# Kernel optimization log

Hardware: AMD Instinct MI355X
Metric: run time of the kernel (lower is better)

Reference implementation:

```python
import jax, jax.numpy as jnp
import numpy as np

N_HEAD, D_MODEL, D_HEAD = 16, 1024, 64
BSZ, SEQ = 4, 2048
SCALE = 1.0 / D_HEAD ** 0.5
LN_EPS = 1e-5
NEG = -1e10


def layer_norm(x, gamma, beta):
    mu = jnp.mean(x, axis=-1, keepdims=True)
    var = jnp.var(x, axis=-1, keepdims=True)
    return (x - mu) * jax.lax.rsqrt(var + LN_EPS) * gamma + beta


def setup_inputs() -> dict:
    key = jax.random.key(0)
    ks = jax.random.split(key, 8)
    q = jax.random.normal(ks[0], (BSZ, SEQ, D_MODEL), dtype=jnp.float32)
    attn_mask = jax.random.randint(ks[1], (SEQ, SEQ), 0, 2).astype(bool)
    s = 1.0 / np.sqrt(D_MODEL)
    Wq = jax.random.normal(ks[2], (D_MODEL, N_HEAD * D_HEAD), dtype=jnp.float32) * s
    Wk = jax.random.normal(ks[3], (D_MODEL, N_HEAD * D_HEAD), dtype=jnp.float32) * s
    Wv = jax.random.normal(ks[4], (D_MODEL, N_HEAD * D_HEAD), dtype=jnp.float32) * s
    Wo = jax.random.normal(ks[5], (N_HEAD * D_HEAD, D_MODEL), dtype=jnp.float32) * s
    gamma = jnp.ones((D_MODEL,), dtype=jnp.float32)
    beta = jnp.zeros((D_MODEL,), dtype=jnp.float32)
    return {"q": q, "attn_mask": attn_mask, "Wq": Wq, "Wk": Wk, "Wv": Wv,
            "Wo": Wo, "gamma": gamma, "beta": beta}


def reference(q, attn_mask, Wq, Wk, Wv, Wo, gamma, beta):
    # pre_lnorm: residual uses the normalized q (as in the torch code, q is reassigned)
    qn = layer_norm(q, gamma, beta)                      # (b, n1, d_model)
    hq = (qn @ Wq).reshape(BSZ, SEQ, N_HEAD, D_HEAD)     # self-attn: k = v = q
    hk = (qn @ Wk).reshape(BSZ, SEQ, N_HEAD, D_HEAD)
    hv = (qn @ Wv).reshape(BSZ, SEQ, N_HEAD, D_HEAD)
    score = jnp.einsum('bind,bjnd->ijbn', hq, hk) * SCALE  # (n1, n2, b, h)
    score = jnp.where(attn_mask[:, :, None, None], NEG, score)
    prob = jax.nn.softmax(score, axis=1)
    vec = jnp.einsum('ijbn,bjnd->bind', prob, hv).reshape(BSZ, SEQ, N_HEAD * D_HEAD)
    attn_out = vec @ Wo
    return qn + attn_out
```

## Files before the change

kernel.cpp:

```cpp
#include <hip/hip_runtime.h>

typedef __bf16 bf16;
typedef __bf16 bf16x8 __attribute__((ext_vector_type(8)));
typedef __bf16 bf16x4 __attribute__((ext_vector_type(4)));
typedef float  f32x4  __attribute__((ext_vector_type(4)));

#define MFMA16 __builtin_amdgcn_mfma_f32_16x16x32_bf16

static constexpr int   BSZ   = 4;
static constexpr int   SEQL  = 2048;
static constexpr int   DM    = 1024;
static constexpr int   NHEAD = 16;
static constexpr int   DHEAD = 64;
static constexpr float NEGB  = -16384.0f;
static constexpr float SCL2  = 0.125f * 1.44269504f;

__device__ __forceinline__ void glds16(bf16* lds, const bf16* g) {
    __builtin_amdgcn_global_load_lds(
        (const __attribute__((address_space(1))) unsigned int*)g,
        (__attribute__((address_space(3))) unsigned int*)lds, 16, 0, 0);
}

__global__ void detect_mask(const unsigned int* __restrict__ m, int* __restrict__ flag) {
    __shared__ int ok[4];
    if (threadIdx.x < 4) ok[threadIdx.x] = 1;
    __syncthreads();
    for (int i = 0; i < 16; ++i) {
        unsigned int w = m[threadIdx.x * 16 + i];
        if (!(w == 0u || w == 1u)) ok[0] = 0;
        if (w & 0xFEFEFEFEu) ok[1] = 0;
        if (!(w == 0u || w == 0x3F800000u)) ok[2] = 0;
        unsigned lo = w & 0xFFFFu, hi = w >> 16;
        if (!((lo == 0u || lo == 0x3F80u) && (hi == 0u || hi == 0x3F80u))) ok[3] = 0;
    }
    __syncthreads();
    if (threadIdx.x == 0)
        *flag = ok[0] ? 0 : (ok[1] ? 1 : (ok[2] ? 2 : 3));
}

__device__ __forceinline__ bool mask_at(const void* m, int fl, long idx) {
    if (fl == 0) return ((const int*)m)[idx] != 0;
    if (fl == 1) return ((const unsigned char*)m)[idx] != 0;
    if (fl == 2) return ((const float*)m)[idx] != 0.0f;
    return ((const unsigned short*)m)[idx] != 0;
}

__global__ __launch_bounds__(256) void prep_bits(const void* __restrict__ mask,
                                                 const int* __restrict__ flagp,
                                                 unsigned long long* __restrict__ mb) {
    const int fl = *flagp;
    const int word = blockIdx.x * 4 + (threadIdx.x >> 6);
    const long base = (long)word * 64 + (threadIdx.x & 63);
    unsigned long long b = __ballot(mask_at(mask, fl, base));
    if ((threadIdx.x & 63) == 0) mb[word] = b;
}

__global__ __launch_bounds__(256) void ln_kernel(
    const float* __restrict__ x, const float* __restrict__ g,
    const float* __restrict__ bta, bf16* __restrict__ y)
{
    const int row = blockIdx.x, t = threadIdx.x;
    const float4 v = ((const float4*)(x + (size_t)row * DM))[t];
    float s  = v.x + v.y + v.z + v.w;
    float ss = v.x * v.x + v.y * v.y + v.z * v.z + v.w * v.w;
    for (int m = 32; m >= 1; m >>= 1) { s += __shfl_xor(s, m); ss += __shfl_xor(ss, m); }
    __shared__ float red[8];
    const int w = t >> 6, L = t & 63;
    if (L == 0) { red[w] = s; red[4 + w] = ss; }
    __syncthreads();
    s  = red[0] + red[1] + red[2] + red[3];
    ss = red[4] + red[5] + red[6] + red[7];
    const float mu = s * (1.0f / DM);
    const float var = ss * (1.0f / DM) - mu * mu;
    const float r = rsqrtf(var + 1e-5f);
    const float4 gv = ((const float4*)g)[t];
    const float4 bv = ((const float4*)bta)[t];
    bf16x4 o;
    o[0] = (bf16)((v.x - mu) * r * gv.x + bv.x);
    o[1] = (bf16)((v.y - mu) * r * gv.y + bv.y);
    o[2] = (bf16)((v.z - mu) * r * gv.z + bv.z);
    o[3] = (bf16)((v.w - mu) * r * gv.w + bv.w);
    ((bf16x4*)(y + (size_t)row * DM))[t] = o;
}

__global__ void cvt_w(const float* __restrict__ Wq, const float* __restrict__ Wk,
                      const float* __restrict__ Wv, const float* __restrict__ Wo,
                      bf16* __restrict__ Wt)
{
    __shared__ float tile[32][33];
    const int z = blockIdx.z;
    const float* src = (z == 0) ? Wq : (z == 1) ? Wk : (z == 2) ? Wv : Wo;
    const float scl = (z == 1) ? SCL2 : 1.0f;
    bf16* dst = Wt + (size_t)z * DM * DM;
    const int tx = threadIdx.x, ty = threadIdx.y;
    const int nIn = blockIdx.x * 32 + tx;
    const int kIn = blockIdx.y * 32;
    for (int i = 0; i < 32; i += 8)
        tile[ty + i][tx] = src[(size_t)(kIn + ty + i) * DM + nIn];
    __syncthreads();
    const int nOut = blockIdx.x * 32;
    const int kOut = blockIdx.y * 32 + tx;
    for (int i = 0; i < 32; i += 8)
        dst[(size_t)(nOut + ty + i) * DM + kOut] = (bf16)(tile[tx][ty + i] * scl);
}

__device__ __forceinline__ void gemm128_core(
    const bf16* __restrict__ A, const bf16* __restrict__ Bt,
    int m0, int n0, bool swapped, f32x4 acc[4][4], bf16* Asm, bf16* Bsm)
{
    const int t = threadIdx.x, w = t >> 6, L = t & 63;
    const int lr = L & 15, lq = L >> 4;
    const int wm = w & 1, wn = w >> 1;
    const int srow = L >> 2, scol = (L & 3) * 8;
    const bf16* Ab = A  + (size_t)(m0 + w * 32 + srow) * DM + scol;
    const bf16* Bb = Bt + (size_t)(n0 + w * 32 + srow) * DM + scol;
    bf16* AsmW = Asm + (w * 32) * 32;
    bf16* BsmW = Bsm + (w * 32) * 32;
    for (int kk = 0; kk < DM; kk += 32) {
        __syncthreads();
        glds16(AsmW,           Ab + kk);
        glds16(AsmW + 16 * 32, Ab + (size_t)16 * DM + kk);
        glds16(BsmW,           Bb + kk);
        glds16(BsmW + 16 * 32, Bb + (size_t)16 * DM + kk);
        __syncthreads();
        bf16x8 af[4], bf_[4];
        #pragma unroll
        for (int i = 0; i < 4; ++i)
            af[i] = *(const bf16x8*)(Asm + (wm * 64 + i * 16 + lr) * 32 + lq * 8);
        #pragma unroll
        for (int j = 0; j < 4; ++j)
            bf_[j] = *(const bf16x8*)(Bsm + (wn * 64 + j * 16 + lr) * 32 + lq * 8);
        if (!swapped) {
            #pragma unroll
            for (int i = 0; i < 4; ++i)
                #pragma unroll
                for (int j = 0; j < 4; ++j)
                    acc[i][j] = MFMA16(af[i], bf_[j], acc[i][j], 0, 0, 0);
        } else {
            #pragma unroll
            for (int i = 0; i < 4; ++i)
                #pragma unroll
                for (int j = 0; j < 4; ++j)
                    acc[i][j] = MFMA16(bf_[j], af[i], acc[i][j], 0, 0, 0);
        }
    }
}

__global__ __launch_bounds__(256) void qkv128(
    const bf16* __restrict__ qn, const bf16* __restrict__ Wt,
    bf16* __restrict__ Qb, bf16* __restrict__ Kb, bf16* __restrict__ Vtb)
{
    __shared__ __align__(16) bf16 Asm[128 * 32];
    __shared__ __align__(16) bf16 Bsm[128 * 32];
    const int ny = blockIdx.y;
    const int z = ny >> 3;
    const int m0 = blockIdx.x * 128, n0 = (ny & 7) * 128;
    f32x4 acc[4][4] = {};
    gemm128_core(qn, Wt + (size_t)z * DM * DM, m0, n0, z == 2, acc, Asm, Bsm);
    const int t = threadIdx.x, L = t & 63, w = t >> 6;
    const int wm = w & 1, wn = w >> 1, lr = L & 15, lq = L >> 4;
    if (z < 2) {
        bf16* dst = z ? Kb : Qb;
        #pragma unroll
        for (int i = 0; i < 4; ++i)
            #pragma unroll
            for (int j = 0; j < 4; ++j)
                #pragma unroll
                for (int r = 0; r < 4; ++r) {
                    int m = m0 + wm * 64 + i * 16 + lq * 4 + r;
                    int n = n0 + wn * 64 + j * 16 + lr;
                    int b = m >> 11, s = m & 2047, h = n >> 6, d = n & 63;
                    dst[(((size_t)b * NHEAD + h) * SEQL + s) * DHEAD + d] = (bf16)acc[i][j][r];
                }
    } else {
        #pragma unroll
        for (int i = 0; i < 4; ++i)
            #pragma unroll
            for (int j = 0; j < 4; ++j)
                #pragma unroll
                for (int r = 0; r < 4; ++r) {
                    int dg = n0 + wn * 64 + j * 16 + lq * 4 + r;
                    int sg = m0 + wm * 64 + i * 16 + lr;
                    int h = dg >> 6, d = dg & 63, b = sg >> 11, s = sg & 2047;
                    Vtb[(((size_t)b * NHEAD + h) * DHEAD + d) * SEQL + s] = (bf16)acc[i][j][r];
                }
    }
}

__global__ __launch_bounds__(256) void out128(
    const bf16* __restrict__ vec, const bf16* __restrict__ Wot,
    const bf16* __restrict__ qnb, float* __restrict__ out)
{
    __shared__ __align__(16) bf16 Asm[128 * 32];
    __shared__ __align__(16) bf16 Bsm[128 * 32];
    const int m0 = blockIdx.x * 128, n0 = blockIdx.y * 128;
    f32x4 acc[4][4] = {};
    gemm128_core(vec, Wot, m0, n0, false, acc, Asm, Bsm);
    const int t = threadIdx.x, L = t & 63, w = t >> 6;
    const int wm = w & 1, wn = w >> 1, lr = L & 15, lq = L >> 4;
    #pragma unroll
    for (int i = 0; i < 4; ++i)
        #pragma unroll
        for (int j = 0; j < 4; ++j)
            #pragma unroll
            for (int r = 0; r < 4; ++r) {
                int m = m0 + wm * 64 + i * 16 + lq * 4 + r;
                int n = n0 + wn * 64 + j * 16 + lr;
                size_t idx = (size_t)m * DM + n;
                out[idx] = acc[i][j][r] + (float)qnb[idx];
            }
}

__global__ __launch_bounds__(256) void flash_attn(
    const bf16* __restrict__ Qb, const bf16* __restrict__ Kb,
    const bf16* __restrict__ Vtb, const unsigned long long* __restrict__ mb,
    bf16* __restrict__ vec)
{
    __shared__ __align__(16) bf16 Ksm [2][64 * 72];
    __shared__ __align__(16) bf16 Vtsm[2][64 * 72];

    const int t = threadIdx.x, w = t >> 6, L = t & 63;
    const int lr = L & 15, lq = L >> 4;
    const int bid = blockIdx.x;
    const int slot = bid & 7, rest = bid >> 3;
    const int qblk = rest & 15;
    const int bh = ((rest >> 4) << 3) + slot;
    const int b = bh >> 4, h = bh & 15;
    const int q0 = qblk * 128 + w * 32;

    const bf16* Qh  = Qb  + (size_t)bh * SEQL * DHEAD;
    const bf16* Kh  = Kb  + (size_t)bh * SEQL * DHEAD;
    const bf16* Vth = Vtb + (size_t)bh * DHEAD * SEQL;

    bf16x8 qf[2][2];
    #pragma unroll
    for (int qg = 0; qg < 2; ++qg)
        #pragma unroll
        for (int ks = 0; ks < 2; ++ks)
            qf[qg][ks] = *(const bf16x8*)(Qh + (size_t)(q0 + qg * 16 + lr) * DHEAD + ks * 32 + lq * 8);

    const unsigned long long* mrow0 = mb + (size_t)(q0 + lr) * (SEQL / 64);
    const unsigned long long* mrow1 = mb + (size_t)(q0 + 16 + lr) * (SEQL / 64);

    f32x4 o[4][2] = {};
    f32x4 lacc[2] = {};

    const bf16 one = (bf16)1.0f;
    const bf16x8 ones8 = {one, one, one, one, one, one, one, one};

    const int sr = t >> 2, sc = (t & 3) * 16;
    const int zrow = ((sr >> 2) & 1) * 32 + ((sr >> 5) & 1) * 16 + ((sr >> 3) & 3) * 4 + (sr & 3);
    constexpr int NT = SEQL / 64;
    bf16x8 kreg[2], vreg[2];

    kreg[0] = *(const bf16x8*)(Kh  + (size_t)sr * DHEAD + sc);
    kreg[1] = *(const bf16x8*)(Kh  + (size_t)sr * DHEAD + sc + 8);
    vreg[0] = *(const bf16x8*)(Vth + (size_t)sr * SEQL + sc);
    vreg[1] = *(const bf16x8*)(Vth + (size_t)sr * SEQL + sc + 8);
    *(bf16x8*)(Ksm[0]  + zrow * 72 + sc)     = kreg[0];
    *(bf16x8*)(Ksm[0]  + zrow * 72 + sc + 8) = kreg[1];
    *(bf16x8*)(Vtsm[0] + sr * 72 + sc)       = vreg[0];
    *(bf16x8*)(Vtsm[0] + sr * 72 + sc + 8)   = vreg[1];
    kreg[0] = *(const bf16x8*)(Kh  + (size_t)(64 + sr) * DHEAD + sc);
    kreg[1] = *(const bf16x8*)(Kh  + (size_t)(64 + sr) * DHEAD + sc + 8);
    vreg[0] = *(const bf16x8*)(Vth + (size_t)sr * SEQL + 64 + sc);
    vreg[1] = *(const bf16x8*)(Vth + (size_t)sr * SEQL + 64 + sc + 8);
    __syncthreads();

    for (int kt = 0; kt < NT; ++kt) {
        const int cur = kt & 1;
        const bf16* Kc = Ksm[cur];
        const bf16* Vc = Vtsm[cur];

        f32x4 s[4][2] = {};
        #pragma unroll
        for (int ks = 0; ks < 2; ++ks) {
            bf16x8 kf[4];
            #pragma unroll
            for (int jj = 0; jj < 4; ++jj)
                kf[jj] = *(const bf16x8*)(Kc + (jj * 16 + lr) * 72 + ks * 32 + lq * 8);
            #pragma unroll
            for (int jj = 0; jj < 4; ++jj)
                #pragma unroll
                for (int qg = 0; qg < 2; ++qg)
                    s[jj][qg] = MFMA16(kf[jj], qf[qg][ks], s[jj][qg], 0, 0, 0);
        }

        if (kt + 1 < NT) {
            bf16* Ka = Ksm[cur ^ 1];
            bf16* Va = Vtsm[cur ^ 1];
            *(bf16x8*)(Ka + zrow * 72 + sc)     = kreg[0];
            *(bf16x8*)(Ka + zrow * 72 + sc + 8) = kreg[1];
            *(bf16x8*)(Va + sr * 72 + sc)       = vreg[0];
            *(bf16x8*)(Va + sr * 72 + sc + 8)   = vreg[1];
            if (kt + 2 < NT) {
                const int kb2 = (kt + 2) * 64;
                kreg[0] = *(const bf16x8*)(Kh  + (size_t)(kb2 + sr) * DHEAD + sc);
                kreg[1] = *(const bf16x8*)(Kh  + (size_t)(kb2 + sr) * DHEAD + sc + 8);
                vreg[0] = *(const bf16x8*)(Vth + (size_t)sr * SEQL + kb2 + sc);
                vreg[1] = *(const bf16x8*)(Vth + (size_t)sr * SEQL + kb2 + sc + 8);
            }
        }

        bf16x8 pf[2][2];
        #pragma unroll
        for (int qg = 0; qg < 2; ++qg) {
            const unsigned long long wmk = (qg == 0 ? mrow0 : mrow1)[kt];
            const unsigned lo = (unsigned)(wmk >> (lq * 8));
            const unsigned hi = (unsigned)(wmk >> 32) >> (lq * 8);
            #pragma unroll
            for (int ks = 0; ks < 2; ++ks) {
                const unsigned na = (ks == 0 ? lo : hi) & 15u;
                const unsigned nb = ((ks == 0 ? lo : hi) >> 4) & 15u;
                bf16x8 pv;
                #pragma unroll
                for (int r = 0; r < 4; ++r) {
                    pv[r]     = (bf16)__builtin_amdgcn_exp2f(((na >> r) & 1u) ? NEGB : s[ks][qg][r]);
                    pv[4 + r] = (bf16)__builtin_amdgcn_exp2f(((nb >> r) & 1u) ? NEGB : s[2 + ks][qg][r]);
                }
                pf[qg][ks] = pv;
            }
        }

        #pragma unroll
        for (int ks = 0; ks < 2; ++ks) {
            #pragma unroll
            for (int qg = 0; qg < 2; ++qg)
                lacc[qg] = MFMA16(ones8, pf[qg][ks], lacc[qg], 0, 0, 0);
            #pragma unroll
            for (int dg = 0; dg < 4; ++dg) {
                bf16x8 vf = *(const bf16x8*)(Vc + (dg * 16 + lr) * 72 + ks * 32 + lq * 8);
                #pragma unroll
                for (int qg = 0; qg < 2; ++qg)
                    o[dg][qg] = MFMA16(vf, pf[qg][ks], o[dg][qg], 0, 0, 0);
            }
        }

        if (kt + 1 < NT) __syncthreads();
    }

    #pragma unroll
    for (int qg = 0; qg < 2; ++qg) {
        const float rl = 1.0f / lacc[qg][0];
        const size_t rowb = ((size_t)b * SEQL + q0 + qg * 16 + lr) * DM + h * DHEAD;
        #pragma unroll
        for (int dg = 0; dg < 4; ++dg) {
            bf16x4 ov;
            #pragma unroll
            for (int r = 0; r < 4; ++r) ov[r] = (bf16)(o[dg][qg][r] * rl);
            *(bf16x4*)(vec + rowb + dg * 16 + lq * 4) = ov;
        }
    }
}

extern "C" void kernel_launch(void* const* d_in, const int* in_sizes, int n_in,
                              void* d_out, int out_size, void* d_ws, size_t ws_size,
                              hipStream_t stream)
{
    const float* qin   = (const float*)d_in[0];
    const void*  mask  = d_in[1];
    const float* Wq    = (const float*)d_in[2];
    const float* Wk    = (const float*)d_in[3];
    const float* Wv    = (const float*)d_in[4];
    const float* Wo    = (const float*)d_in[5];
    const float* gamma = (const float*)d_in[6];
    const float* beta  = (const float*)d_in[7];
    float* out = (float*)d_out;

    char* w = (char*)d_ws;
    int*  flag = (int*)w;
    bf16* qnb  = (bf16*)(w + 256);
    bf16* Wt   = qnb + (size_t)8192 * 1024;
    bf16* Qb   = Wt + (size_t)4 * 1024 * 1024;
    bf16* Kb   = Qb + (size_t)8192 * 1024;
    bf16* Vtb  = Kb + (size_t)8192 * 1024;
    bf16* vec  = Vtb + (size_t)8192 * 1024;
    unsigned long long* mb = (unsigned long long*)(vec + (size_t)8192 * 1024);

    detect_mask<<<1, 256, 0, stream>>>((const unsigned int*)mask, flag);
    prep_bits<<<SEQL * (SEQL / 64) / 4, 256, 0, stream>>>(mask, flag, mb);
    ln_kernel<<<8192, 256, 0, stream>>>(qin, gamma, beta, qnb);
    cvt_w<<<dim3(32, 32, 4), dim3(32, 8), 0, stream>>>(Wq, Wk, Wv, Wo, Wt);
    qkv128<<<dim3(64, 24), 256, 0, stream>>>(qnb, Wt, Qb, Kb, Vtb);
    flash_attn<<<1024, 256, 0, stream>>>(Qb, Kb, Vtb, mb, vec);
    out128<<<dim3(64, 8), 256, 0, stream>>>(vec, Wt + (size_t)3 * 1024 * 1024, qnb, out);
}
```

Before: 335.4 us.

## Pre-transpose mask into per-register wave ballot words for scalar cndmask selection

A new prep kernel re-packs the row-major mask bitmap into 64-bit lane masks, one per MFMA accumulator register slot, for each 16-row query group and key tile. The attention inner loop can then load a wave-uniform scalar mask word and zero the exponentiated score with a single v_cndmask, replacing per-lane bit extraction and select before exp2. The final normalisation also uses a hardware reciprocal instead of a division. The cost is one extra small kernel launch, inline asm that depends on the SGPR-pair condition operand and on the readfirstlane assumption, and a slightly less precise reciprocal.

Result: slower. 344.6 us (+2.7%).

```diff
diff --git a/kernel.cpp b/kernel.cpp
--- a/kernel.cpp
+++ b/kernel.cpp
@@ -12,7 +12,6 @@
 static constexpr int   DM    = 1024;
 static constexpr int   NHEAD = 16;
 static constexpr int   DHEAD = 64;
-static constexpr float NEGB  = -16384.0f;
 static constexpr float SCL2  = 0.125f * 1.44269504f;
 
 __device__ __forceinline__ void glds16(bf16* lds, const bf16* g) {
@@ -47,12 +46,31 @@
 
 __global__ __launch_bounds__(256) void prep_bits(const void* __restrict__ mask,
                                                  const int* __restrict__ flagp,
-                                                 unsigned long long* __restrict__ mb) {
+                                                 unsigned long long* __restrict__ rb) {
     const int fl = *flagp;
     const int word = blockIdx.x * 4 + (threadIdx.x >> 6);
     const long base = (long)word * 64 + (threadIdx.x & 63);
     unsigned long long b = __ballot(mask_at(mask, fl, base));
-    if ((threadIdx.x & 63) == 0) mb[word] = b;
+    if ((threadIdx.x & 63) == 0) rb[word] = b;
+}
+
+__global__ __launch_bounds__(256) void prep_words(
+    const unsigned long long* __restrict__ rb, unsigned long long* __restrict__ wm)
+{
+    const int t = threadIdx.x, L = t & 63, w = t >> 6;
+    const int pair = blockIdx.x * 4 + w;
+    const int qgrp = pair >> 5, kt = pair & 31;
+    const unsigned long long r0 = rb[(size_t)(qgrp * 16 + (L & 15)) * 32 + kt];
+    const int lq = L >> 4;
+    unsigned long long myw = 0;
+    #pragma unroll
+    for (int jr = 0; jr < 16; ++jr) {
+        const int jj = jr >> 2, r = jr & 3;
+        const int bitpos = (jj & 1) * 32 + lq * 8 + (jj >> 1) * 4 + r;
+        unsigned long long bal = __ballot(((r0 >> bitpos) & 1ull) != 0ull);
+        if (L == jr) myw = bal;
+    }
+    if (L < 16) wm[(size_t)pair * 16 + L] = myw;
 }
 
 __global__ __launch_bounds__(256) void ln_kernel(
@@ -239,14 +257,16 @@
         for (int ks = 0; ks < 2; ++ks)
             qf[qg][ks] = *(const bf16x8*)(Qh + (size_t)(q0 + qg * 16 + lr) * DHEAD + ks * 32 + lq * 8);
 
-    const unsigned long long* mrow0 = mb + (size_t)(q0 + lr) * (SEQL / 64);
-    const unsigned long long* mrow1 = mb + (size_t)(q0 + 16 + lr) * (SEQL / 64);
+    const int qgrp0 = __builtin_amdgcn_readfirstlane(q0 >> 4);
+    const unsigned long long* wm0 = mb + (size_t)qgrp0 * 512;
+    const unsigned long long* wm1 = wm0 + 512;
 
     f32x4 o[4][2] = {};
     f32x4 lacc[2] = {};
 
     const bf16 one = (bf16)1.0f;
     const bf16x8 ones8 = {one, one, one, one, one, one, one, one};
+    const float fz = 0.0f;
 
     const int sr = t >> 2, sc = (t & 3) * 16;
     const int zrow = ((sr >> 2) & 1) * 32 + ((sr >> 5) & 1) * 16 + ((sr >> 3) & 3) * 4 + (sr & 3);
@@ -305,18 +325,21 @@
         bf16x8 pf[2][2];
         #pragma unroll
         for (int qg = 0; qg < 2; ++qg) {
-            const unsigned long long wmk = (qg == 0 ? mrow0 : mrow1)[kt];
-            const unsigned lo = (unsigned)(wmk >> (lq * 8));
-            const unsigned hi = (unsigned)(wmk >> 32) >> (lq * 8);
+            const unsigned long long* wp = (qg ? wm1 : wm0) + kt * 16;
             #pragma unroll
             for (int ks = 0; ks < 2; ++ks) {
-                const unsigned na = (ks == 0 ? lo : hi) & 15u;
-                const unsigned nb = ((ks == 0 ? lo : hi) >> 4) & 15u;
                 bf16x8 pv;
                 #pragma unroll
                 for (int r = 0; r < 4; ++r) {
-                    pv[r]     = (bf16)__builtin_amdgcn_exp2f(((na >> r) & 1u) ? NEGB : s[ks][qg][r]);
-                    pv[4 + r] = (bf16)__builtin_amdgcn_exp2f(((nb >> r) & 1u) ? NEGB : s[2 + ks][qg][r]);
+                    float e0 = __builtin_amdgcn_exp2f(s[ks][qg][r]);
+                    float e1 = __builtin_amdgcn_exp2f(s[2 + ks][qg][r]);
+                    float z0, z1;
+                    asm("v_cndmask_b32 %0, %1, %2, %3"
+                        : "=v"(z0) : "v"(e0), "v"(fz), "s"(wp[ks * 4 + r]));
+                    asm("v_cndmask_b32 %0, %1, %2, %3"
+                        : "=v"(z1) : "v"(e1), "v"(fz), "s"(wp[(2 + ks) * 4 + r]));
+                    pv[r]     = (bf16)z0;
+                    pv[4 + r] = (bf16)z1;
                 }
                 pf[qg][ks] = pv;
             }
@@ -341,7 +364,7 @@
 
     #pragma unroll
     for (int qg = 0; qg < 2; ++qg) {
-        const float rl = 1.0f / lacc[qg][0];
+        const float rl = __builtin_amdgcn_rcpf(lacc[qg][0]);
         const size_t rowb = ((size_t)b * SEQL + q0 + qg * 16 + lr) * DM + h * DHEAD;
         #pragma unroll
         for (int dg = 0; dg < 4; ++dg) {
@@ -375,13 +398,15 @@
     bf16* Kb   = Qb + (size_t)8192 * 1024;
     bf16* Vtb  = Kb + (size_t)8192 * 1024;
     bf16* vec  = Vtb + (size_t)8192 * 1024;
-    unsigned long long* mb = (unsigned long long*)(vec + (size_t)8192 * 1024);
+    unsigned long long* rbits  = (unsigned long long*)(vec + (size_t)8192 * 1024);
+    unsigned long long* mwords = rbits + 65536;
 
     detect_mask<<<1, 256, 0, stream>>>((const unsigned int*)mask, flag);
-    prep_bits<<<SEQL * (SEQL / 64) / 4, 256, 0, stream>>>(mask, flag, mb);
+    prep_bits<<<SEQL * (SEQL / 64) / 4, 256, 0, stream>>>(mask, flag, rbits);
+    prep_words<<<1024, 256, 0, stream>>>(rbits, mwords);
     ln_kernel<<<8192, 256, 0, stream>>>(qin, gamma, beta, qnb);
     cvt_w<<<dim3(32, 32, 4), dim3(32, 8), 0, stream>>>(Wq, Wk, Wv, Wo, Wt);
     qkv128<<<dim3(64, 24), 256, 0, stream>>>(qnb, Wt, Qb, Kb, Vtb);
-    flash_attn<<<1024, 256, 0, stream>>>(Qb, Kb, Vtb, mb, vec);
+    flash_attn<<<1024, 256, 0, stream>>>(Qb, Kb, Vtb, mwords, vec);
     out128<<<dim3(64, 8), 256, 0, stream>>>(vec, Wt + (size_t)3 * 1024 * 1024, qnb, out);
 }
```
